# Performance work log

Hardware: AMD Instinct MI355X
Metric: run time of the kernel (lower is better)

## Reference

```python
import jax, jax.numpy as jnp
import numpy as np

B, S, D, H, DC, HC = 2, 2048, 1024, 16, 64, 16  # batch, seq, hidden, heads, coord_dim, head_coord_dim
HD = D // H  # head_dim


def setup_inputs() -> dict:
    key = jax.random.key(0)
    ks = jax.random.split(key, 12)
    s = lambda fan_in: 1.0 / np.sqrt(fan_in)
    return {
        "hidden_states": jax.random.normal(ks[0], (B, S, D), jnp.float32),
        "coordinates": jax.random.normal(ks[1], (B, S, DC), jnp.float32),
        # weights stored [in, out] (used as x @ W + b, equivalent to torch Linear)
        "Wv": jax.random.uniform(ks[2], (D, D), jnp.float32, -s(D), s(D)),
        "bv": jax.random.uniform(ks[3], (D,), jnp.float32, -s(D), s(D)),
        "Wc": jax.random.uniform(ks[4], (DC, H * HC), jnp.float32, -s(DC), s(DC)),
        "bc": jax.random.uniform(ks[5], (H * HC,), jnp.float32, -s(DC), s(DC)),
        "Wn": jax.random.uniform(ks[6], (DC, DC), jnp.float32, -s(DC), s(DC)),
        "bn": jax.random.uniform(ks[7], (DC,), jnp.float32, -s(DC), s(DC)),
        "Wo": jax.random.uniform(ks[8], (D, D), jnp.float32, -s(D), s(D)),
        "bo": jax.random.uniform(ks[9], (D,), jnp.float32, -s(D), s(D)),
        "gamma": jax.random.normal(ks[10], (1, H, 1, 1), jnp.float32),
    }


def reference(hidden_states, coordinates, Wv, bv, Wc, bc, Wn, bn, Wo, bo, gamma):
    b, s, _ = hidden_states.shape
    # value: [B,H,S,HD]
    value = (hidden_states @ Wv + bv).reshape(b, s, H, HD).transpose(0, 2, 1, 3)
    # coord heads: [B,H,S,HC]
    z = (coordinates @ Wc + bc).reshape(b, s, H, HC).transpose(0, 2, 1, 3)
    z_sq = jnp.sum(z * z, axis=-1, keepdims=True)  # [B,H,S,1]
    sq_dist = z_sq + jnp.swapaxes(z_sq, -1, -2) - 2.0 * jnp.einsum("bhsc,bhtc->bhst", z, z)
    sq_dist = jnp.maximum(sq_dist, 0.0)
    g = jax.nn.softplus(gamma)  # [1,H,1,1]
    attn = jax.nn.softmax(-g * sq_dist, axis=-1)  # [B,H,S,S]
    out = jnp.einsum("bhst,bhtd->bhsd", attn, value)
    out = out.transpose(0, 2, 1, 3).reshape(b, s, D)
    updated_hidden = out @ Wo + bo
    updated_coords = coordinates @ Wn + bn
    return (updated_hidden, updated_coords)
```

## Files before the change

kernel.cpp:

```cpp
#include <hip/hip_runtime.h>
#include <hip/hip_bf16.h>

typedef short bf16x8 __attribute__((ext_vector_type(8)));
typedef float f32x4 __attribute__((ext_vector_type(4)));
typedef float f32x16 __attribute__((ext_vector_type(16)));
typedef unsigned short u16;
typedef unsigned int u32;

__device__ __forceinline__ u16 f2b(float f) {
  __hip_bfloat16 h = __float2bfloat16(f);
  return *reinterpret_cast<u16*>(&h);
}

#define MFMA16(a, b, c) __builtin_amdgcn_mfma_f32_16x16x32_bf16((a), (b), (c), 0, 0, 0)
#define MFMA32(a, b, c) __builtin_amdgcn_mfma_f32_32x32x16_bf16((a), (b), (c), 0, 0, 0)


__global__ void k_cvt(const float* __restrict__ in, u16* __restrict__ out, int n) {
  int i = (blockIdx.x * 256 + threadIdx.x) * 4;
  if (i >= n) return;
  float4 v = *reinterpret_cast<const float4*>(in + i);
  ushort4 o;
  o.x = f2b(v.x); o.y = f2b(v.y); o.z = f2b(v.z); o.w = f2b(v.w);
  *reinterpret_cast<ushort4*>(out + i) = o;
}

__global__ void k_wT(const float* __restrict__ W, u16* __restrict__ WT) {
  __shared__ float t[64][65];
  int tid = threadIdx.x;
  int r0 = (blockIdx.x & 15) << 6;
  int c0 = (blockIdx.x >> 4) << 6;
#pragma unroll
  for (int rep = 0; rep < 4; ++rep) {
    int e = tid + rep * 256;
    int r = e >> 4, c4 = (e & 15) << 2;
    float4 v = *reinterpret_cast<const float4*>(W + (size_t)(r0 + r) * 1024 + c0 + c4);
    t[r][c4] = v.x; t[r][c4 + 1] = v.y; t[r][c4 + 2] = v.z; t[r][c4 + 3] = v.w;
  }
  __syncthreads();
#pragma unroll
  for (int rep = 0; rep < 4; ++rep) {
    int e = tid + rep * 256;
    int c = e >> 4, r4 = (e & 15) << 2;
    ushort4 o;
    o.x = f2b(t[r4][c]); o.y = f2b(t[r4 + 1][c]);
    o.z = f2b(t[r4 + 2][c]); o.w = f2b(t[r4 + 3][c]);
    *reinterpret_cast<ushort4*>(WT + (size_t)(c0 + c) * 1024 + r0 + r4) = o;
  }
}

__global__ void k_z(const float* __restrict__ C, const float* __restrict__ Wc,
                    const float* __restrict__ bc, const float* __restrict__ gamma,
                    u16* __restrict__ Z, u16* __restrict__ Zg, u32* __restrict__ zghl) {
  int gid = blockIdx.x * 256 + threadIdx.x;
  int bs = gid >> 4, h = gid & 15;
  float gm = gamma[h];
  float g = (gm > 15.f) ? gm : log1pf(__expf(gm));
  float g2 = g * 1.4426950408889634f;
  float tg2 = 2.f * g2;
  const float* crow = C + (size_t)bs * 64;
  float acc[16];
#pragma unroll
  for (int c = 0; c < 16; ++c) acc[c] = bc[h * 16 + c];
  for (int k = 0; k < 64; ++k) {
    float cv = crow[k];
    const float* wr = Wc + (size_t)k * 256 + h * 16;
#pragma unroll
    for (int c = 0; c < 16; ++c) acc[c] = fmaf(cv, wr[c], acc[c]);
  }
  float sq = 0.f;
  u16 tz[16], tg[16];
#pragma unroll
  for (int c = 0; c < 16; ++c) {
    sq += acc[c] * acc[c];
    tz[c] = f2b(acc[c]);
    tg[c] = f2b(tg2 * acc[c]);
  }
  float x = -g2 * sq;
  u32 xu = __float_as_uint(x);
  float xh = __uint_as_float(xu & 0xFFFF0000u);
  u32 packed = (xu >> 16) | ((u32)f2b(x - xh) << 16);
  int b = bs >> 11, s = bs & 2047;
  int bh = (b << 4) + h;
  size_t ro = (((size_t)bh << 11) + s) * 16;
  *reinterpret_cast<uint4*>(Z + ro) = *reinterpret_cast<uint4*>(tz);
  *reinterpret_cast<uint4*>(Z + ro + 8) = *reinterpret_cast<uint4*>(tz + 8);
  *reinterpret_cast<uint4*>(Zg + ro) = *reinterpret_cast<uint4*>(tg);
  *reinterpret_cast<uint4*>(Zg + ro + 8) = *reinterpret_cast<uint4*>(tg + 8);
  zghl[((size_t)bh << 11) + s] = packed;
}

__global__ void k_coords(const float* __restrict__ C, const float* __restrict__ Wn,
                         const float* __restrict__ bn, float* __restrict__ out) {
  int gid = blockIdx.x * 256 + threadIdx.x;
  int bs = gid >> 6, c = gid & 63;
  const float* crow = C + (size_t)bs * 64;
  float acc = bn[c];
#pragma unroll 8
  for (int k = 0; k < 64; ++k) acc = fmaf(crow[k], Wn[k * 64 + c], acc);
  out[gid] = acc;
}

template <int OUTM>
__global__ __launch_bounds__(512, 4) void k_gemm(const u16* __restrict__ A,
                                                 const u16* __restrict__ BT,
                                                 const float* __restrict__ bias,
                                                 void* __restrict__ Cout,
                                                 int M, int N, int K) {
  __shared__ u16 As[2][128 * 64];
  __shared__ u16 Bs[2][64 * 64];
  int nbn = N >> 6;
  int bm = blockIdx.x / nbn, bn = blockIdx.x % nbn;
  int tid = threadIdx.x, lane = tid & 63, w = tid >> 6;
  int wm = w >> 1, wn = w & 1;
  int l15 = lane & 15, lg = lane >> 4;
  int lr = lane >> 3;
  int swc = (lane & 7) ^ lr;

  f32x4 acc[2][2];
#pragma unroll
  for (int mi = 0; mi < 2; ++mi)
#pragma unroll
    for (int ni = 0; ni < 2; ++ni) acc[mi][ni] = (f32x4){0.f, 0.f, 0.f, 0.f};

  const u16* Abase = A + (size_t)(bm * 128 + w * 8 + lr) * K + swc * 8;
  const u16* Bbase = BT + (size_t)(bn * 64 + w * 8 + lr) * K + swc * 8;
  int rsw = l15 & 7;

#define GSTAGE(BUF, KK)                                                             \
  do {                                                                              \
    __builtin_amdgcn_global_load_lds(                                               \
        (const __attribute__((address_space(1))) u32*)(Abase + (KK)),               \
        (__attribute__((address_space(3))) u32*)&As[(BUF)][(w * 8) * 64], 16, 0, 0);\
    __builtin_amdgcn_global_load_lds(                                               \
        (const __attribute__((address_space(1))) u32*)(Abase + (size_t)64 * K + (KK)),\
        (__attribute__((address_space(3))) u32*)&As[(BUF)][(64 + w * 8) * 64], 16, 0, 0);\
    __builtin_amdgcn_global_load_lds(                                               \
        (const __attribute__((address_space(1))) u32*)(Bbase + (KK)),               \
        (__attribute__((address_space(3))) u32*)&Bs[(BUF)][(w * 8) * 64], 16, 0, 0);\
  } while (0)

  const int nk = K >> 6;
  GSTAGE(0, 0);
  for (int it = 0; it < nk; ++it) {
    int cur = it & 1;
    if (it + 1 < nk) {
      GSTAGE(cur ^ 1, (it + 1) * 64);
      asm volatile("s_waitcnt vmcnt(3)" ::: "memory");
    } else {
      asm volatile("s_waitcnt vmcnt(0)" ::: "memory");
    }
    __builtin_amdgcn_sched_barrier(0);
    __builtin_amdgcn_s_barrier();
#pragma unroll
    for (int kk = 0; kk < 2; ++kk) {
      int ch = (kk * 4 + lg) ^ rsw;
      bf16x8 af[2], bfr[2];
#pragma unroll
      for (int mi = 0; mi < 2; ++mi)
        af[mi] = *reinterpret_cast<const bf16x8*>(&As[cur][(wm * 32 + mi * 16 + l15) * 64 + ch * 8]);
#pragma unroll
      for (int ni = 0; ni < 2; ++ni)
        bfr[ni] = *reinterpret_cast<const bf16x8*>(&Bs[cur][(wn * 32 + ni * 16 + l15) * 64 + ch * 8]);
#pragma unroll
      for (int mi = 0; mi < 2; ++mi)
#pragma unroll
        for (int ni = 0; ni < 2; ++ni)
          acc[mi][ni] = MFMA16(af[mi], bfr[ni], acc[mi][ni]);
    }
    __builtin_amdgcn_sched_barrier(0);
    __builtin_amdgcn_s_barrier();
  }
#undef GSTAGE

#pragma unroll
  for (int mi = 0; mi < 2; ++mi) {
#pragma unroll
    for (int ni = 0; ni < 2; ++ni) {
      int col = bn * 64 + wn * 32 + ni * 16 + l15;
      float bv = bias[col];
      if (OUTM == 0) {
#pragma unroll
        for (int j = 0; j < 4; ++j) {
          int row = bm * 128 + wm * 32 + mi * 16 + lg * 4 + j;
          reinterpret_cast<float*>(Cout)[(size_t)row * N + col] = acc[mi][ni][j] + bv;
        }
      } else {
        int row0 = bm * 128 + wm * 32 + mi * 16 + lg * 4;
        int b = row0 >> 11, tg = (row0 >> 4) & 127;
        int hi_ = lg >> 1, jb = (lg & 1) << 2;
        int h = col >> 6, hd = col & 63, dh = hd >> 5, lv = hd & 31;
        size_t addr = ((((size_t)(b * 16 + h) * 128 + tg) * 2 + dh) << 9) +
                      ((hi_ * 32 + lv) << 3) + jb;
        ushort4 o;
        o.x = f2b(acc[mi][ni][0] + bv); o.y = f2b(acc[mi][ni][1] + bv);
        o.z = f2b(acc[mi][ni][2] + bv); o.w = f2b(acc[mi][ni][3] + bv);
        *reinterpret_cast<ushort4*>(reinterpret_cast<u16*>(Cout) + addr) = o;
      }
    }
  }
}

__global__ __launch_bounds__(256, 2) void k_attn(const u16* __restrict__ Z,
                                                 const u16* __restrict__ Zg,
                                                 const u32* __restrict__ zghl,
                                                 const u16* __restrict__ VF,
                                                 u16* __restrict__ O) {
  __shared__ __align__(16) char smem[33792];
  float* psqf = reinterpret_cast<float*>(smem + 32768);

  int tid = threadIdx.x, lane = tid & 63, w = tid >> 6;
  int l31 = lane & 31, hi = lane >> 5;
  int hi4 = hi << 2, hi8 = hi << 3;
  int th = w & 1, qh = w >> 1, th32 = th << 5;
  int bh = blockIdx.x >> 4, qt = blockIdx.x & 15;
  int q0 = qt << 7;
  int h = bh & 15, bb = bh >> 4;

  const u16* Zb = Z + ((size_t)bh << 11) * 16;
  const u16* Zgb = Zg + ((size_t)bh << 11) * 16;
  const u32* ghl = zghl + ((size_t)bh << 11);
  const u16* VFb = VF + ((size_t)bh << 17);

  int qx0 = (qh << 6) + l31;
  int qx1 = qx0 + 32;

  bf16x8 zq2_0 = *reinterpret_cast<const bf16x8*>(Zgb + (size_t)(q0 + qx0) * 16 + hi8);
  bf16x8 zq2_1 = *reinterpret_cast<const bf16x8*>(Zgb + (size_t)(q0 + qx1) * 16 + hi8);

  u32 gq0 = ghl[q0 + qx0], gq1 = ghl[q0 + qx1];
  uint4 ab0 = {0x3F803F80u, gq0, 0u, 0u};
  uint4 ab1 = {0x3F803F80u, gq1, 0u, 0u};
  if (hi) { ab0.x = 0u; ab0.y = 0u; ab1.x = 0u; ab1.y = 0u; }
  bf16x8 aug_b0 = *reinterpret_cast<bf16x8*>(&ab0);
  bf16x8 aug_b1 = *reinterpret_cast<bf16x8*>(&ab1);

  uint4 aqu = {0u, 0x3F803F80u, 0u, 0u};
  if (hi) aqu.y = 0u;
  bf16x8 aug_q = *reinterpret_cast<bf16x8*>(&aqu);
  f32x16 qpart0 = MFMA32(aug_q, aug_b0, (f32x16){});
  f32x16 qpart1 = MFMA32(aug_q, aug_b1, (f32x16){});

  const u16* zap = Zb + (size_t)(th32 + l31) * 16 + hi8;
  const u32* xtp = ghl + th32 + l31;
  const u16* vwp = VFb + ((size_t)th << 11) + ((size_t)lane << 3);

  f32x16 oacc00 = {}, oacc01 = {}, oacc10 = {}, oacc11 = {};
  f32x4 ps0 = {}, ps1 = {};

  int swz = (l31 ^ (l31 >> 2)) & 3;
  char* pbase = smem + (w << 12) + l31 * 64;

  bf16x8 zA_c = *reinterpret_cast<const bf16x8*>(zap);
  u32 zhl_c = xtp[0];

#pragma unroll 2
  for (int tt = 0; tt < 32; ++tt) {
    const int t0 = tt << 6;
    const u16* vtb = vwp + (tt << 12);
    bf16x8 vb00 = *reinterpret_cast<const bf16x8*>(vtb);
    bf16x8 vb01 = *reinterpret_cast<const bf16x8*>(vtb + 512);
    bf16x8 vb10 = *reinterpret_cast<const bf16x8*>(vtb + 1024);
    bf16x8 vb11 = *reinterpret_cast<const bf16x8*>(vtb + 1536);
    bf16x8 zA_n = zA_c;
    u32 zhl_n = zhl_c;
    if (tt < 31) {
      zA_n = *reinterpret_cast<const bf16x8*>(zap + (size_t)(t0 + 64) * 16);
      zhl_n = xtp[t0 + 64];
    }

    uint4 aau = {hi ? 0u : zhl_c, 0u, 0u, 0u};
    bf16x8 aug_a = *reinterpret_cast<bf16x8*>(&aau);

    f32x16 sc0 = MFMA32(aug_a, aug_b0, qpart0);
    sc0 = MFMA32(zA_c, zq2_0, sc0);
    f32x16 sc1 = MFMA32(aug_a, aug_b1, qpart1);
    sc1 = MFMA32(zA_c, zq2_1, sc1);

    char* pb = pbase + ((tt & 1) << 14);
#pragma unroll
    for (int g = 0; g < 4; ++g) {
      int cb = ((g ^ swz) << 4) + (hi << 3);
      {
        float e0 = fminf(sc0[g * 4 + 0], 0.f), e1 = fminf(sc0[g * 4 + 1], 0.f);
        float e2 = fminf(sc0[g * 4 + 2], 0.f), e3 = fminf(sc0[g * 4 + 3], 0.f);
        float p0 = __builtin_amdgcn_exp2f(e0), p1 = __builtin_amdgcn_exp2f(e1);
        float p2 = __builtin_amdgcn_exp2f(e2), p3 = __builtin_amdgcn_exp2f(e3);
        ps0[0] += p0; ps0[1] += p1; ps0[2] += p2; ps0[3] += p3;
        u32 pk0, pk1;
        asm("v_cvt_pk_bf16_f32 %0, %1, %2" : "=v"(pk0) : "v"(p0), "v"(p1));
        asm("v_cvt_pk_bf16_f32 %0, %1, %2" : "=v"(pk1) : "v"(p2), "v"(p3));
        uint2 pkv = {pk0, pk1};
        *reinterpret_cast<uint2*>(pb + cb) = pkv;
      }
      {
        float e0 = fminf(sc1[g * 4 + 0], 0.f), e1 = fminf(sc1[g * 4 + 1], 0.f);
        float e2 = fminf(sc1[g * 4 + 2], 0.f), e3 = fminf(sc1[g * 4 + 3], 0.f);
        float p0 = __builtin_amdgcn_exp2f(e0), p1 = __builtin_amdgcn_exp2f(e1);
        float p2 = __builtin_amdgcn_exp2f(e2), p3 = __builtin_amdgcn_exp2f(e3);
        ps1[0] += p0; ps1[1] += p1; ps1[2] += p2; ps1[3] += p3;
        u32 pk0, pk1;
        asm("v_cvt_pk_bf16_f32 %0, %1, %2" : "=v"(pk0) : "v"(p0), "v"(p1));
        asm("v_cvt_pk_bf16_f32 %0, %1, %2" : "=v"(pk1) : "v"(p2), "v"(p3));
        uint2 pkv = {pk0, pk1};
        *reinterpret_cast<uint2*>(pb + 2048 + cb) = pkv;
      }
    }

    int c0b = (((0 * 2 + hi) ^ swz) << 4);
    int c1b = (((1 * 2 + hi) ^ swz) << 4);
    bf16x8 pa00 = *reinterpret_cast<const bf16x8*>(pb + c0b);
    bf16x8 pa01 = *reinterpret_cast<const bf16x8*>(pb + c1b);
    bf16x8 pa10 = *reinterpret_cast<const bf16x8*>(pb + 2048 + c0b);
    bf16x8 pa11 = *reinterpret_cast<const bf16x8*>(pb + 2048 + c1b);

    __builtin_amdgcn_s_setprio(1);
    oacc00 = MFMA32(pa00, vb00, oacc00);
    oacc01 = MFMA32(pa00, vb01, oacc01);
    oacc10 = MFMA32(pa10, vb00, oacc10);
    oacc11 = MFMA32(pa10, vb01, oacc11);
    oacc00 = MFMA32(pa01, vb10, oacc00);
    oacc01 = MFMA32(pa01, vb11, oacc01);
    oacc10 = MFMA32(pa11, vb10, oacc10);
    oacc11 = MFMA32(pa11, vb11, oacc11);
    __builtin_amdgcn_s_setprio(0);

    zA_c = zA_n; zhl_c = zhl_n;
  }

  float psum0 = (ps0[0] + ps0[1]) + (ps0[2] + ps0[3]);
  float psum1 = (ps1[0] + ps1[1]) + (ps1[2] + ps1[3]);
  psum0 += __shfl_xor(psum0, 32, 64);
  psum1 += __shfl_xor(psum1, 32, 64);

  __syncthreads();
  if (th == 1) {
    char* dst = smem + ((w >> 1) << 14) + lane * 16;
#pragma unroll
    for (int r = 0; r < 4; ++r) {
      *reinterpret_cast<f32x4*>(dst + (0 + r) * 1024) =
          (f32x4){oacc00[r * 4], oacc00[r * 4 + 1], oacc00[r * 4 + 2], oacc00[r * 4 + 3]};
      *reinterpret_cast<f32x4*>(dst + (4 + r) * 1024) =
          (f32x4){oacc01[r * 4], oacc01[r * 4 + 1], oacc01[r * 4 + 2], oacc01[r * 4 + 3]};
      *reinterpret_cast<f32x4*>(dst + (8 + r) * 1024) =
          (f32x4){oacc10[r * 4], oacc10[r * 4 + 1], oacc10[r * 4 + 2], oacc10[r * 4 + 3]};
      *reinterpret_cast<f32x4*>(dst + (12 + r) * 1024) =
          (f32x4){oacc11[r * 4], oacc11[r * 4 + 1], oacc11[r * 4 + 2], oacc11[r * 4 + 3]};
    }
  }
  if (lane < 32) {
    psqf[(w * 2 + 0) * 32 + l31] = psum0;
    psqf[(w * 2 + 1) * 32 + l31] = psum1;
  }
  __syncthreads();
  if (th == 0) {
    const char* src = smem + ((w >> 1) << 14) + lane * 16;
#pragma unroll
    for (int r = 0; r < 4; ++r) {
      f32x4 v0 = *reinterpret_cast<const f32x4*>(src + (0 + r) * 1024);
      f32x4 v1 = *reinterpret_cast<const f32x4*>(src + (4 + r) * 1024);
      f32x4 v2 = *reinterpret_cast<const f32x4*>(src + (8 + r) * 1024);
      f32x4 v3 = *reinterpret_cast<const f32x4*>(src + (12 + r) * 1024);
#pragma unroll
      for (int j = 0; j < 4; ++j) {
        oacc00[r * 4 + j] += v0[j];
        oacc01[r * 4 + j] += v1[j];
        oacc10[r * 4 + j] += v2[j];
        oacc11[r * 4 + j] += v3[j];
      }
    }
#pragma unroll
    for (int qbk = 0; qbk < 2; ++qbk) {
#pragma unroll
      for (int g = 0; g < 4; ++g) {
        f32x4 a = *reinterpret_cast<const f32x4*>(&psqf[(w * 2 + qbk) * 32 + (g << 3) + hi4]);
        f32x4 b2 = *reinterpret_cast<const f32x4*>(&psqf[((w + 1) * 2 + qbk) * 32 + (g << 3) + hi4]);
#pragma unroll
        for (int j = 0; j < 4; ++j) {
          float inv = __builtin_amdgcn_rcpf(a[j] + b2[j]);
          int qrow = (g << 3) + hi4 + j;
          int srow = q0 + (qh << 6) + (qbk << 5) + qrow;
          u16* orow = O + ((size_t)(bb * 2048 + srow) << 10) + h * 64 + l31;
          float v0 = (qbk ? oacc10[g * 4 + j] : oacc00[g * 4 + j]);
          float v1 = (qbk ? oacc11[g * 4 + j] : oacc01[g * 4 + j]);
          orow[0] = f2b(v0 * inv);
          orow[32] = f2b(v1 * inv);
        }
      }
    }
  }
}

extern "C" void kernel_launch(void* const* d_in, const int* in_sizes, int n_in,
                              void* d_out, int out_size, void* d_ws, size_t ws_size,
                              hipStream_t stream) {
  const float* hs     = (const float*)d_in[0];
  const float* coords = (const float*)d_in[1];
  const float* Wv     = (const float*)d_in[2];
  const float* bv     = (const float*)d_in[3];
  const float* Wc     = (const float*)d_in[4];
  const float* bc     = (const float*)d_in[5];
  const float* Wn     = (const float*)d_in[6];
  const float* bn     = (const float*)d_in[7];
  const float* Wo     = (const float*)d_in[8];
  const float* bo     = (const float*)d_in[9];
  const float* gamma  = (const float*)d_in[10];
  float* out_h = (float*)d_out;
  float* out_c = out_h + 4194304;

  char* ws = (char*)d_ws;
  u16*   HSb  = (u16*)(ws + 0);
  u16*   O    = (u16*)(ws + 0);
  u16*   WvT  = (u16*)(ws + 8388608);
  u16*   WoT  = (u16*)(ws + 10485760);
  u16*   Zw   = (u16*)(ws + 12582912);
  u16*   Zgw  = (u16*)(ws + 14680064);
  u32*   zghl = (u32*)(ws + 16777216);
  u16*   VFw  = (u16*)(ws + 17039360);

  k_cvt<<<4096, 256, 0, stream>>>(hs, HSb, 4194304);
  k_wT<<<256, 256, 0, stream>>>(Wv, WvT);
  k_wT<<<256, 256, 0, stream>>>(Wo, WoT);
  k_z<<<256, 256, 0, stream>>>(coords, Wc, bc, gamma, Zw, Zgw, zghl);
  k_gemm<1><<<512, 512, 0, stream>>>(HSb, WvT, bv, VFw, 4096, 1024, 1024);
  k_attn<<<512, 256, 0, stream>>>(Zw, Zgw, zghl, VFw, O);
  k_gemm<0><<<512, 512, 0, stream>>>(O, WoT, bo, out_h, 4096, 1024, 1024);
  k_coords<<<1024, 256, 0, stream>>>(coords, Wn, bn, out_c);
}
```

Measured before the change: 110.3 us.

## Enlarge GEMM tile to 128x128 and switch to 32x32x16 MFMA

The projection GEMMs now use a 128x128 output tile per block instead of 128x64, which halves the block count to 256. Each warp computes a 32x64 sub-tile with two 32x32x16 MFMAs in place of four 16x16x32 MFMAs. The goal is more reuse of operands loaded into LDS and fewer LDS reads per FLOP. In exchange the LDS footprint doubles, occupancy drops (launch bounds 512,2), only 256 blocks cover the CUs, and the epilogue index maps are rewritten for the 32x32 accumulator layout.

```diff
diff --git a/kernel.cpp b/kernel.cpp
--- a/kernel.cpp
+++ b/kernel.cpp
@@ -102,42 +102,41 @@
 }
 
 template <int OUTM>
-__global__ __launch_bounds__(512, 4) void k_gemm(const u16* __restrict__ A,
+__global__ __launch_bounds__(512, 2) void k_gemm(const u16* __restrict__ A,
                                                  const u16* __restrict__ BT,
                                                  const float* __restrict__ bias,
                                                  void* __restrict__ Cout,
                                                  int M, int N, int K) {
   __shared__ u16 As[2][128 * 64];
-  __shared__ u16 Bs[2][64 * 64];
-  int nbn = N >> 6;
+  __shared__ u16 Bs[2][128 * 64];
+  int nbn = N >> 7;
   int bm = blockIdx.x / nbn, bn = blockIdx.x % nbn;
   int tid = threadIdx.x, lane = tid & 63, w = tid >> 6;
   int wm = w >> 1, wn = w & 1;
-  int l15 = lane & 15, lg = lane >> 4;
+  int l31 = lane & 31, hi = lane >> 5;
   int lr = lane >> 3;
   int swc = (lane & 7) ^ lr;
-
-  f32x4 acc[2][2];
-#pragma unroll
-  for (int mi = 0; mi < 2; ++mi)
-#pragma unroll
-    for (int ni = 0; ni < 2; ++ni) acc[mi][ni] = (f32x4){0.f, 0.f, 0.f, 0.f};
+  int rsw = l31 & 7;
+
+  f32x16 acc0 = {}, acc1 = {};
 
   const u16* Abase = A + (size_t)(bm * 128 + w * 8 + lr) * K + swc * 8;
-  const u16* Bbase = BT + (size_t)(bn * 64 + w * 8 + lr) * K + swc * 8;
-  int rsw = l15 & 7;
-
-#define GSTAGE(BUF, KK)                                                             \
-  do {                                                                              \
-    __builtin_amdgcn_global_load_lds(                                               \
-        (const __attribute__((address_space(1))) u32*)(Abase + (KK)),               \
-        (__attribute__((address_space(3))) u32*)&As[(BUF)][(w * 8) * 64], 16, 0, 0);\
-    __builtin_amdgcn_global_load_lds(                                               \
+  const u16* Bbase = BT + (size_t)(bn * 128 + w * 8 + lr) * K + swc * 8;
+
+#define GSTAGE(BUF, KK)                                                               \
+  do {                                                                                \
+    __builtin_amdgcn_global_load_lds(                                                 \
+        (const __attribute__((address_space(1))) u32*)(Abase + (KK)),                 \
+        (__attribute__((address_space(3))) u32*)&As[(BUF)][(w * 8) * 64], 16, 0, 0);  \
+    __builtin_amdgcn_global_load_lds(                                                 \
         (const __attribute__((address_space(1))) u32*)(Abase + (size_t)64 * K + (KK)),\
         (__attribute__((address_space(3))) u32*)&As[(BUF)][(64 + w * 8) * 64], 16, 0, 0);\
-    __builtin_amdgcn_global_load_lds(                                               \
-        (const __attribute__((address_space(1))) u32*)(Bbase + (KK)),               \
-        (__attribute__((address_space(3))) u32*)&Bs[(BUF)][(w * 8) * 64], 16, 0, 0);\
+    __builtin_amdgcn_global_load_lds(                                                 \
+        (const __attribute__((address_space(1))) u32*)(Bbase + (KK)),                 \
+        (__attribute__((address_space(3))) u32*)&Bs[(BUF)][(w * 8) * 64], 16, 0, 0);  \
+    __builtin_amdgcn_global_load_lds(                                                 \
+        (const __attribute__((address_space(1))) u32*)(Bbase + (size_t)64 * K + (KK)),\
+        (__attribute__((address_space(3))) u32*)&Bs[(BUF)][(64 + w * 8) * 64], 16, 0, 0);\
   } while (0)
 
   const int nk = K >> 6;
@@ -146,27 +145,20 @@
     int cur = it & 1;
     if (it + 1 < nk) {
       GSTAGE(cur ^ 1, (it + 1) * 64);
-      asm volatile("s_waitcnt vmcnt(3)" ::: "memory");
+      asm volatile("s_waitcnt vmcnt(4)" ::: "memory");
     } else {
       asm volatile("s_waitcnt vmcnt(0)" ::: "memory");
     }
     __builtin_amdgcn_sched_barrier(0);
     __builtin_amdgcn_s_barrier();
 #pragma unroll
-    for (int kk = 0; kk < 2; ++kk) {
-      int ch = (kk * 4 + lg) ^ rsw;
-      bf16x8 af[2], bfr[2];
-#pragma unroll
-      for (int mi = 0; mi < 2; ++mi)
-        af[mi] = *reinterpret_cast<const bf16x8*>(&As[cur][(wm * 32 + mi * 16 + l15) * 64 + ch * 8]);
-#pragma unroll
-      for (int ni = 0; ni < 2; ++ni)
-        bfr[ni] = *reinterpret_cast<const bf16x8*>(&Bs[cur][(wn * 32 + ni * 16 + l15) * 64 + ch * 8]);
-#pragma unroll
-      for (int mi = 0; mi < 2; ++mi)
-#pragma unroll
-        for (int ni = 0; ni < 2; ++ni)
-          acc[mi][ni] = MFMA16(af[mi], bfr[ni], acc[mi][ni]);
+    for (int s = 0; s < 4; ++s) {
+      int ch = (s * 2 + hi) ^ rsw;
+      bf16x8 af = *reinterpret_cast<const bf16x8*>(&As[cur][(wm * 32 + l31) * 64 + ch * 8]);
+      bf16x8 bf0 = *reinterpret_cast<const bf16x8*>(&Bs[cur][(wn * 64 + l31) * 64 + ch * 8]);
+      bf16x8 bf1 = *reinterpret_cast<const bf16x8*>(&Bs[cur][(wn * 64 + 32 + l31) * 64 + ch * 8]);
+      acc0 = MFMA32(af, bf0, acc0);
+      acc1 = MFMA32(af, bf1, acc1);
     }
     __builtin_amdgcn_sched_barrier(0);
     __builtin_amdgcn_s_barrier();
@@ -174,27 +166,28 @@
 #undef GSTAGE
 
 #pragma unroll
-  for (int mi = 0; mi < 2; ++mi) {
-#pragma unroll
-    for (int ni = 0; ni < 2; ++ni) {
-      int col = bn * 64 + wn * 32 + ni * 16 + l15;
-      float bv = bias[col];
-      if (OUTM == 0) {
-#pragma unroll
-        for (int j = 0; j < 4; ++j) {
-          int row = bm * 128 + wm * 32 + mi * 16 + lg * 4 + j;
-          reinterpret_cast<float*>(Cout)[(size_t)row * N + col] = acc[mi][ni][j] + bv;
-        }
-      } else {
-        int row0 = bm * 128 + wm * 32 + mi * 16 + lg * 4;
-        int b = row0 >> 11, tg = (row0 >> 4) & 127;
-        int hi_ = lg >> 1, jb = (lg & 1) << 2;
-        int h = col >> 6, hd = col & 63, dh = hd >> 5, lv = hd & 31;
+  for (int nj = 0; nj < 2; ++nj) {
+    const f32x16 a = nj ? acc1 : acc0;
+    int col = bn * 128 + wn * 64 + nj * 32 + l31;
+    float bv = bias[col];
+    if (OUTM == 0) {
+#pragma unroll
+      for (int j = 0; j < 16; ++j) {
+        int row = bm * 128 + wm * 32 + (j & 3) + 4 * hi + 8 * (j >> 2);
+        reinterpret_cast<float*>(Cout)[(size_t)row * N + col] = a[j] + bv;
+      }
+    } else {
+      int h = col >> 6, hd = col & 63, dh = hd >> 5, lv = hd & 31;
+#pragma unroll
+      for (int q = 0; q < 4; ++q) {
+        int vrow = bm * 128 + wm * 32 + 4 * hi + 8 * q;
+        int b = vrow >> 11, tg = (vrow >> 4) & 127;
+        int hi_ = (vrow >> 3) & 1, jj0 = vrow & 7;
         size_t addr = ((((size_t)(b * 16 + h) * 128 + tg) * 2 + dh) << 9) +
-                      ((hi_ * 32 + lv) << 3) + jb;
+                      ((hi_ * 32 + lv) << 3) + jj0;
         ushort4 o;
-        o.x = f2b(acc[mi][ni][0] + bv); o.y = f2b(acc[mi][ni][1] + bv);
-        o.z = f2b(acc[mi][ni][2] + bv); o.w = f2b(acc[mi][ni][3] + bv);
+        o.x = f2b(a[q * 4 + 0] + bv); o.y = f2b(a[q * 4 + 1] + bv);
+        o.z = f2b(a[q * 4 + 2] + bv); o.w = f2b(a[q * 4 + 3] + bv);
         *reinterpret_cast<ushort4*>(reinterpret_cast<u16*>(Cout) + addr) = o;
       }
     }
@@ -422,8 +415,8 @@
   k_wT<<<256, 256, 0, stream>>>(Wv, WvT);
   k_wT<<<256, 256, 0, stream>>>(Wo, WoT);
   k_z<<<256, 256, 0, stream>>>(coords, Wc, bc, gamma, Zw, Zgw, zghl);
-  k_gemm<1><<<512, 512, 0, stream>>>(HSb, WvT, bv, VFw, 4096, 1024, 1024);
+  k_gemm<1><<<256, 512, 0, stream>>>(HSb, WvT, bv, VFw, 4096, 1024, 1024);
   k_attn<<<512, 256, 0, stream>>>(Zw, Zgw, zghl, VFw, O);
-  k_gemm<0><<<512, 512, 0, stream>>>(O, WoT, bo, out_h, 4096, 1024, 1024);
+  k_gemm<0><<<256, 512, 0, stream>>>(O, WoT, bo, out_h, 4096, 1024, 1024);
   k_coords<<<1024, 256, 0, stream>>>(coords, Wn, bn, out_c);
 }
```

Result: slower. 119.0 us (+7.9%).
